# Performance work log

Measured on AMD Instinct MI355X. Metric: run time of the kernel, lower is better.

Reference implementation:

```python
import jax, jax.numpy as jnp
import numpy as np

B, N, E, D, H, C, FF, NQ, NCLS = 4, 1024, 512, 256, 2, 128, 1024, 4, 24
K_LOCAL, K_GLOBAL = 8, 7


def _ln(x, g, b, eps=1e-5):
    m = jnp.mean(x, -1, keepdims=True)
    v = jnp.mean((x - m) ** 2, -1, keepdims=True)
    return (x - m) * jax.lax.rsqrt(v + eps) * g + b


def _knn_mask(dist, k, exclude_self):
    # dist: [n, n]; returns bool mask[target, source] of k nearest sources per target
    n = dist.shape[-1]
    d = jnp.where(jnp.eye(n, dtype=bool), 1e9, dist) if exclude_self else dist
    idx = jax.lax.top_k(-d, k)[1]  # [n, k]
    rows = jnp.arange(n)[:, None]
    return jnp.zeros((n, n), dtype=bool).at[rows, idx].set(True)


def _mha(q, k, v, scale, extra_mask=None):
    # q: [B,Lq,H,C]  k,v: [B,Lk,H,C]
    logits = jnp.einsum('bqhc,bkhc->bhqk', q, k) * scale
    if extra_mask is not None:
        logits = logits + extra_mask
    a = jax.nn.softmax(logits, axis=-1)
    return jnp.einsum('bhqk,bkhc->bqhc', a, v)


def _forward(inputs, cellposes, sparse_rand, emb_W, emb_b, pe_tab, pe_W1, pe_b1, pe_W2, pe_b2,
             gat_W, gat_att_src, gat_att_dst, gat_b, ln_g, ln_b,
             tf_qkv_W, tf_qkv_b, tf_out_W, tf_out_b, tf_ff1_W, tf_ff1_b, tf_ff2_W, tf_ff2_b,
             tf_ln1_g, tf_ln1_b, tf_ln2_g, tf_ln2_b,
             query_embed, pool_in_W, pool_in_b, pool_out_W, pool_out_b,
             m1_W, m1_b, m_ln1_g, m_ln1_b, m2_W, m2_b, m_ln2_g, m_ln2_b, m3_W, m3_b,
             c1_W, c1_b, c2_W, c2_b, c3_W, c3_b, c4_W, c4_b, masks):
    # masks are all ones (full bags) -> key_padding_mask is all-False, no padding effect
    x = inputs @ emb_W.T + emb_b                                  # [B,N,D]
    # 2D position embedding: per-coordinate Embedding -> Linear -> ReLU -> Linear
    pos_idx = jnp.clip(cellposes, 0, 1000).astype(jnp.int32)      # [B,N,2]
    pes = []
    for c in range(2):
        e = pe_tab[c][pos_idx[..., c]]                            # [B,N,D//2]
        e = jax.nn.relu(e @ pe_W1[c].T + pe_b1[c]) @ pe_W2[c].T + pe_b2[c]
        pes.append(e)
    x = x + jnp.concatenate(pes, axis=-1)
    # kNN graph: local k=8 with self-loops + global k=7 without; coalesce('max') => edge-set union
    pm = cellposes.mean(axis=1, keepdims=True)
    ps = cellposes.std(axis=1, keepdims=True) + 1e-8
    pn = (cellposes - pm) / ps
    sq = jnp.sum((pn[:, :, None, :] - pn[:, None, :, :]) ** 2, axis=-1)
    dist = jax.lax.stop_gradient(jnp.sqrt(sq + 1e-12))            # [B,N,N]
    local = jax.vmap(lambda d: _knn_mask(d, K_LOCAL, False))(dist)
    glob = jax.vmap(lambda d: _knn_mask(d, K_GLOBAL, True))(dist)
    adj = local | glob                                            # [B, target, source]
    # GAT layers (PyG GATConv; edge weights are ignored since edge_dim=None)
    for l in range(gat_W.shape[0]):
        res = x
        h = (x @ gat_W[l].T).reshape(B, N, H, C)
        a_src = jnp.einsum('bnhc,hc->bnh', h, gat_att_src[l])
        a_dst = jnp.einsum('bnhc,hc->bnh', h, gat_att_dst[l])
        e = jax.nn.leaky_relu(a_dst[:, :, None, :] + a_src[:, None, :, :], 0.2)  # [B,t,s,H]
        e = jnp.where(adj[..., None], e, -1e9)
        a = jax.nn.softmax(e, axis=2)
        out = jnp.einsum('btsh,bshc->bthc', a, h).reshape(B, N, D) + gat_b[l]
        x = _ln(out + res, ln_g, ln_b)
    # TransformerEncoder: post-norm, ReLU FFN, batch_first, eval (no dropout)
    scale = 1.0 / jnp.sqrt(jnp.float32(C))
    for l in range(tf_qkv_W.shape[0]):
        qkv = x @ tf_qkv_W[l].T + tf_qkv_b[l]
        q, k, v = [t.reshape(B, N, H, C) for t in jnp.split(qkv, 3, axis=-1)]
        o = _mha(q, k, v, scale).reshape(B, N, D) @ tf_out_W[l].T + tf_out_b[l]
        x = _ln(x + o, tf_ln1_g[l], tf_ln1_b[l])
        ff = jax.nn.relu(x @ tf_ff1_W[l].T + tf_ff1_b[l]) @ tf_ff2_W[l].T + tf_ff2_b[l]
        x = _ln(x + ff, tf_ln2_g[l], tf_ln2_b[l])
    x = _ln(x, ln_g, ln_b)
    pooled_avg = x.mean(axis=1)                                   # AdaptiveAvgPool1d(1) == mean over seq
    # Sparse multihead attention pooling with learned queries
    queries = jnp.broadcast_to(query_embed[None], (B, NQ, D))
    attn_mask = jnp.where(sparse_rand < 0.3, 0.0, -1e9)           # [NQ, N]
    Wq, Wk, Wv = jnp.split(pool_in_W, 3, axis=0)
    bq, bk, bv = jnp.split(pool_in_b, 3, axis=0)
    q = (queries @ Wq.T + bq).reshape(B, NQ, H, C)
    k = (x @ Wk.T + bk).reshape(B, N, H, C)
    v = (x @ Wv.T + bv).reshape(B, N, H, C)
    pooled_att = _mha(q, k, v, scale, attn_mask[None, None]).reshape(B, NQ, D) @ pool_out_W.T + pool_out_b
    combined = jnp.concatenate([pooled_avg, pooled_att.reshape(B, NQ * D)], axis=-1)  # [B,(1+NQ)*D]
    h = jax.nn.relu(combined @ m1_W.T + m1_b)
    h = _ln(h, m_ln1_g, m_ln1_b)
    h = jax.nn.relu(h @ m2_W.T + m2_b)
    h = _ln(h, m_ln2_g, m_ln2_b)
    h = h @ m3_W.T + m3_b
    h = jax.nn.relu(h @ c1_W.T + c1_b)
    h = jax.nn.relu(h @ c2_W.T + c2_b)
    h = jax.nn.relu(h @ c3_W.T + c3_b)
    return h @ c4_W.T + c4_b                                      # [B, num_classes]


def setup_inputs() -> dict:
    key = jax.random.key(0)
    ks = iter(jax.random.split(key, 80))
    def W(shape, s=0.02):
        return jax.random.normal(next(ks), shape, jnp.float32) * s
    z = lambda *s: jnp.zeros(s, jnp.float32)
    o = lambda *s: jnp.ones(s, jnp.float32)
    return dict(
        inputs=jax.random.normal(next(ks), (B, N, E), jnp.float32),
        cellposes=jax.random.uniform(next(ks), (B, N, 2), jnp.float32) * 1000.0,
        sparse_rand=jax.random.uniform(next(ks), (NQ, N), jnp.float32),
        emb_W=W((D, E)), emb_b=z(D),
        pe_tab=W((2, 1001, D // 2)), pe_W1=W((2, D // 2, D // 2)), pe_b1=z(2, D // 2),
        pe_W2=W((2, D // 2, D // 2)), pe_b2=z(2, D // 2),
        gat_W=W((2, D, D)), gat_att_src=W((2, H, C)), gat_att_dst=W((2, H, C)), gat_b=z(2, D),
        ln_g=o(D), ln_b=z(D),
        tf_qkv_W=W((2, 3 * D, D)), tf_qkv_b=z(2, 3 * D), tf_out_W=W((2, D, D)), tf_out_b=z(2, D),
        tf_ff1_W=W((2, FF, D)), tf_ff1_b=z(2, FF), tf_ff2_W=W((2, D, FF)), tf_ff2_b=z(2, D),
        tf_ln1_g=o(2, D), tf_ln1_b=z(2, D), tf_ln2_g=o(2, D), tf_ln2_b=z(2, D),
        query_embed=W((NQ, D)),
        pool_in_W=W((3 * D, D)), pool_in_b=z(3 * D), pool_out_W=W((D, D)), pool_out_b=z(D),
        m1_W=W((1024, (1 + NQ) * D)), m1_b=z(1024), m_ln1_g=o(1024), m_ln1_b=z(1024),
        m2_W=W((1024, 1024)), m2_b=z(1024), m_ln2_g=o(1024), m_ln2_b=z(1024),
        m3_W=W((1024, 1024)), m3_b=z(1024),
        c1_W=W((1032, 1024)), c1_b=z(1032), c2_W=W((512, 1032)), c2_b=z(512),
        c3_W=W((256, 512)), c3_b=z(256), c4_W=W((NCLS, 256)), c4_b=z(NCLS),
        masks=jnp.ones((B, N), jnp.int32),
    )


def reference(inputs, cellposes, sparse_rand, emb_W, emb_b, pe_tab, pe_W1, pe_b1, pe_W2, pe_b2,
              gat_W, gat_att_src, gat_att_dst, gat_b, ln_g, ln_b,
              tf_qkv_W, tf_qkv_b, tf_out_W, tf_out_b, tf_ff1_W, tf_ff1_b, tf_ff2_W, tf_ff2_b,
              tf_ln1_g, tf_ln1_b, tf_ln2_g, tf_ln2_b,
              query_embed, pool_in_W, pool_in_b, pool_out_W, pool_out_b,
              m1_W, m1_b, m_ln1_g, m_ln1_b, m2_W, m2_b, m_ln2_g, m_ln2_b, m3_W, m3_b,
              c1_W, c1_b, c2_W, c2_b, c3_W, c3_b, c4_W, c4_b, masks):
    return _forward(inputs, cellposes, sparse_rand, emb_W, emb_b, pe_tab, pe_W1, pe_b1, pe_W2, pe_b2,
                    gat_W, gat_att_src, gat_att_dst, gat_b, ln_g, ln_b,
                    tf_qkv_W, tf_qkv_b, tf_out_W, tf_out_b, tf_ff1_W, tf_ff1_b, tf_ff2_W, tf_ff2_b,
                    tf_ln1_g, tf_ln1_b, tf_ln2_g, tf_ln2_b,
                    query_embed, pool_in_W, pool_in_b, pool_out_W, pool_out_b,
                    m1_W, m1_b, m_ln1_g, m_ln1_b, m2_W, m2_b, m_ln2_g, m_ln2_b, m3_W, m3_b,
                    c1_W, c1_b, c2_W, c2_b, c3_W, c3_b, c4_W, c4_b, masks)
```

## Files before the change

### kernel.cpp

```cpp
#include <hip/hip_runtime.h>
#include <hip/hip_bf16.h>


typedef __bf16 bf16x8 __attribute__((ext_vector_type(8)));
typedef float  f32x4  __attribute__((ext_vector_type(4)));

__device__ __forceinline__ ushort f2b(float f) {
  __hip_bfloat16 h = __float2bfloat16(f);
  return *(ushort*)&h;
}
__device__ __forceinline__ float b2f(ushort u) {
  union { unsigned i; float f; } v; v.i = ((unsigned)u) << 16; return v.f;
}

__device__ __forceinline__ float blk_sum256(float v, float* red) {
  int t = threadIdx.x;
  red[t] = v; __syncthreads();
  #pragma unroll
  for (int off = 128; off > 0; off >>= 1) {
    if (t < off) red[t] += red[t + off];
    __syncthreads();
  }
  float r = red[0]; __syncthreads();
  return r;
}

__device__ __forceinline__ void stage8(const ushort* __restrict__ src, ushort* dst) {
  *(uint4*)dst = *(const uint4*)src;
}
__device__ __forceinline__ void stage8(const float* __restrict__ src, ushort* dst) {
  float4 a = ((const float4*)src)[0];
  float4 b = ((const float4*)src)[1];
  ushort4 o0, o1;
  o0.x = f2b(a.x); o0.y = f2b(a.y); o0.z = f2b(a.z); o0.w = f2b(a.w);
  o1.x = f2b(b.x); o1.y = f2b(b.y); o1.z = f2b(b.z); o1.w = f2b(b.w);
  *(ushort4*)dst = o0;
  *(ushort4*)(dst + 4) = o1;
}

template<typename CT, typename AT, typename WT, bool VSPLIT, bool GATS, bool AMERGE>
__global__ __launch_bounds__(256) void mfma_gemm(
    const AT* __restrict__ A, int lda,
    const WT* __restrict__ Bw, int ldb,
    const float* __restrict__ bias,
    CT* __restrict__ C, int ldc, int K, int relu,
    ushort* __restrict__ VT,
    const float* __restrict__ asrcW, const float* __restrict__ adstW,
    float* __restrict__ ASRC, float* __restrict__ ADST,
    const float* __restrict__ Mp, const float* __restrict__ Lp)
{
  __shared__ ushort As[64][40];
  __shared__ ushort Bs[128][40];
  int tid = threadIdx.x;
  int lane = tid & 63, wave = tid >> 6;
  int wm = wave >> 1, wn = wave & 1;
  int quad = lane >> 4, l16 = lane & 15;
  long mBase = blockIdx.y * 64, nBase = blockIdx.x * 128;

  float aw0 = 0.f, aw1 = 0.f, ainv = 0.f;
  int ap_lrow = 0, ap_qt = 0, ap_b = 0;
  if constexpr (AMERGE) {
    int r = tid >> 2;
    long gm = mBase + r;
    ap_b = (int)(gm >> 10);
    int nn = (int)(gm & 1023);
    ap_qt = nn >> 6;
    ap_lrow = nn & 63;
  }

  f32x4 zero4 = {0.f, 0.f, 0.f, 0.f};
  f32x4 acc[2][4];
  #pragma unroll
  for (int i = 0; i < 2; i++)
    #pragma unroll
    for (int j = 0; j < 4; j++) acc[i][j] = zero4;

  for (int k0 = 0; k0 < K; k0 += 32) {
    if constexpr (AMERGE) {
      int r = tid >> 2, sg = (tid & 3) * 8;
      int col = k0 + sg;
      int hh = col >> 7, cc = col & 127;
      int bh = ap_b * 2 + hh;
      int p0 = (ap_qt * 2 + 0) * 8 + bh;
      int p1 = (ap_qt * 2 + 1) * 8 + bh;
      float m0 = Mp[p0 * 64 + ap_lrow], m1 = Mp[p1 * 64 + ap_lrow];
      float l0 = Lp[p0 * 64 + ap_lrow], l1 = Lp[p1 * 64 + ap_lrow];
      float mm2 = fmaxf(m0, m1);
      float w0 = expf(m0 - mm2), w1 = expf(m1 - mm2);
      float inv = 1.f / (w0 * l0 + w1 * l1);
      const ushort* o0 = (const ushort*)A + ((long)(p0 * 64 + ap_lrow)) * 128 + cc;
      const ushort* o1 = (const ushort*)A + ((long)(p1 * 64 + ap_lrow)) * 128 + cc;
      ushort* dst = &As[r][sg];
      #pragma unroll
      for (int i = 0; i < 8; i++)
        dst[i] = f2b((w0 * b2f(o0[i]) + w1 * b2f(o1[i])) * inv);
    } else {
      int r = tid >> 2, sg = (tid & 3) * 8;
      stage8(A + (mBase + r) * lda + k0 + sg, &As[r][sg]);
    }
    #pragma unroll
    for (int p = 0; p < 2; p++) {
      int idx = p * 256 + tid;
      int r = idx >> 2, sg = (idx & 3) * 8;
      stage8(Bw + (nBase + r) * ldb + k0 + sg, &Bs[r][sg]);
    }
    __syncthreads();
    bf16x8 af[2], bfr[4];
    #pragma unroll
    for (int i = 0; i < 2; i++)
      af[i] = *(const bf16x8*)&As[wm * 32 + i * 16 + l16][quad * 8];
    #pragma unroll
    for (int j = 0; j < 4; j++)
      bfr[j] = *(const bf16x8*)&Bs[wn * 64 + j * 16 + l16][quad * 8];
    #pragma unroll
    for (int i = 0; i < 2; i++)
      #pragma unroll
      for (int j = 0; j < 4; j++)
        acc[i][j] = __builtin_amdgcn_mfma_f32_16x16x32_bf16(af[i], bfr[j], acc[i][j], 0, 0, 0);
    __syncthreads();
  }
  #pragma unroll
  for (int i = 0; i < 2; i++) {
    #pragma unroll
    for (int j = 0; j < 4; j++) {
      long col = nBase + wn * 64 + j * 16 + l16;
      float bv = bias ? bias[col] : 0.f;
      long row0 = mBase + wm * 32 + i * 16 + quad * 4;
      if (VSPLIT && col >= 512) {
        int cm = (int)col - 512, hh = cm >> 7, cc = cm & 127;
        long bidx = row0 >> 10, n0 = row0 & 1023;
        ushort4 o;
        o.x = f2b(acc[i][j][0] + bv);
        o.y = f2b(acc[i][j][1] + bv);
        o.z = f2b(acc[i][j][2] + bv);
        o.w = f2b(acc[i][j][3] + bv);
        *(ushort4*)&VT[(((bidx * 2 + hh) * 128 + cc) << 10) + n0] = o;
      } else {
        #pragma unroll
        for (int r = 0; r < 4; r++) {
          float v = acc[i][j][r] + bv;
          if (relu) v = fmaxf(v, 0.f);
          if constexpr (sizeof(CT) == 2) C[(row0 + r) * ldc + col] = f2b(v);
          else                           C[(row0 + r) * ldc + col] = v;
        }
      }
    }
  }
  if constexpr (GATS) {
    __shared__ float RS[64][2], RD[64][2];
    float ps[2][4], pd[2][4];
    #pragma unroll
    for (int i = 0; i < 2; i++)
      #pragma unroll
      for (int r = 0; r < 4; r++) { ps[i][r] = 0.f; pd[i][r] = 0.f; }
    #pragma unroll
    for (int j = 0; j < 4; j++) {
      long col = nBase + wn * 64 + j * 16 + l16;
      float ws = asrcW[col], wd = adstW[col];
      #pragma unroll
      for (int i = 0; i < 2; i++)
        #pragma unroll
        for (int r = 0; r < 4; r++) {
          ps[i][r] += acc[i][j][r] * ws;
          pd[i][r] += acc[i][j][r] * wd;
        }
    }
    #pragma unroll
    for (int off = 1; off < 16; off <<= 1)
      #pragma unroll
      for (int i = 0; i < 2; i++)
        #pragma unroll
        for (int r = 0; r < 4; r++) {
          ps[i][r] += __shfl_xor(ps[i][r], off);
          pd[i][r] += __shfl_xor(pd[i][r], off);
        }
    if (l16 == 0) {
      #pragma unroll
      for (int i = 0; i < 2; i++)
        #pragma unroll
        for (int r = 0; r < 4; r++) {
          int row = wm * 32 + i * 16 + quad * 4 + r;
          RS[row][wn] = ps[i][r];
          RD[row][wn] = pd[i][r];
        }
    }
    __syncthreads();
    if (tid < 64) {
      long gr = mBase + tid;
      ASRC[gr * 2 + blockIdx.x] = RS[tid][0] + RS[tid][1];
      ADST[gr * 2 + blockIdx.x] = RD[tid][0] + RD[tid][1];
    }
  }
}

template<typename CT, typename AT, typename WT>
static void mgemm(hipStream_t st, const AT* A, int lda, const WT* B, int ldb,
                  const float* bias, CT* C, int ldc, int M, int N, int K, int relu) {
  dim3 grid(N / 128, M / 64);
  mfma_gemm<CT, AT, WT, false, false, false><<<grid, 256, 0, st>>>(
      A, lda, B, ldb, bias, C, ldc, K, relu,
      nullptr, nullptr, nullptr, nullptr, nullptr, nullptr, nullptr);
}
template<typename AT, typename WT>
static void mgemm_vt(hipStream_t st, const AT* A, int lda, const WT* B, int ldb,
                     const float* bias, ushort* C, int ldc, int M, int N, int K, ushort* VT) {
  dim3 grid(N / 128, M / 64);
  mfma_gemm<ushort, AT, WT, true, false, false><<<grid, 256, 0, st>>>(
      A, lda, B, ldb, bias, C, ldc, K, 0, VT,
      nullptr, nullptr, nullptr, nullptr, nullptr, nullptr);
}
template<typename AT, typename WT>
static void mgemm_gat(hipStream_t st, const AT* A, int lda, const WT* B, int ldb,
                      float* C, int ldc, int M, int N, int K,
                      const float* asrcW, const float* adstW, float* AS, float* AD) {
  dim3 grid(N / 128, M / 64);
  mfma_gemm<float, AT, WT, false, true, false><<<grid, 256, 0, st>>>(
      A, lda, B, ldb, nullptr, C, ldc, K, 0, nullptr,
      asrcW, adstW, AS, AD, nullptr, nullptr);
}
template<typename WT>
static void mgemm_amrg(hipStream_t st, const ushort* OP, const float* Mp, const float* Lp,
                       const WT* B, int ldb, const float* bias,
                       float* C, int ldc, int M, int N, int K) {
  dim3 grid(N / 128, M / 64);
  mfma_gemm<float, ushort, WT, false, false, true><<<grid, 256, 0, st>>>(
      OP, 0, B, ldb, bias, C, ldc, K, 0, nullptr,
      nullptr, nullptr, nullptr, nullptr, Mp, Lp);
}

__global__ __launch_bounds__(256) void pos_mlp(
    const float* __restrict__ cellp, const float* __restrict__ tab,
    const float* __restrict__ W1, const float* __restrict__ b1,
    const float* __restrict__ W2, const float* __restrict__ b2,
    float* __restrict__ X, ushort* __restrict__ Xb)
{
  __shared__ ushort Es[64][136];
  __shared__ ushort Bs[128][136];
  __shared__ ushort H1s[64][136];
  int tid = threadIdx.x;
  int lane = tid & 63, wave = tid >> 6;
  int wm = wave >> 1, wn = wave & 1;
  int quad = lane >> 4, l16 = lane & 15;
  int r0 = blockIdx.x * 64, c = blockIdx.y;

  #pragma unroll
  for (int p = 0; p < 4; p++) {
    int idx = p * 256 + tid;
    int r = idx >> 4, c8 = (idx & 15) * 8;
    float pos = cellp[(r0 + r) * 2 + c];
    pos = fminf(fmaxf(pos, 0.f), 1000.f);
    int pi = (int)pos;
    stage8(tab + ((long)(c * 1001 + pi)) * 128 + c8, &Es[r][c8]);
  }
  #pragma unroll
  for (int p = 0; p < 8; p++) {
    int idx = p * 256 + tid;
    int r = idx >> 4, c8 = (idx & 15) * 8;
    stage8(W1 + ((long)(c * 128 + r)) * 128 + c8, &Bs[r][c8]);
  }
  __syncthreads();

  f32x4 zero4 = {0.f, 0.f, 0.f, 0.f};
  f32x4 acc[2][4];
  #pragma unroll
  for (int i = 0; i < 2; i++)
    #pragma unroll
    for (int j = 0; j < 4; j++) acc[i][j] = zero4;
  #pragma unroll
  for (int ks = 0; ks < 4; ks++) {
    bf16x8 af[2], bfr[4];
    #pragma unroll
    for (int i = 0; i < 2; i++)
      af[i] = *(const bf16x8*)&Es[wm * 32 + i * 16 + l16][ks * 32 + quad * 8];
    #pragma unroll
    for (int j = 0; j < 4; j++)
      bfr[j] = *(const bf16x8*)&Bs[wn * 64 + j * 16 + l16][ks * 32 + quad * 8];
    #pragma unroll
    for (int i = 0; i < 2; i++)
      #pragma unroll
      for (int j = 0; j < 4; j++)
        acc[i][j] = __builtin_amdgcn_mfma_f32_16x16x32_bf16(af[i], bfr[j], acc[i][j], 0, 0, 0);
  }
  #pragma unroll
  for (int i = 0; i < 2; i++)
    #pragma unroll
    for (int j = 0; j < 4; j++) {
      int col = wn * 64 + j * 16 + l16;
      float bv = b1[c * 128 + col];
      #pragma unroll
      for (int r = 0; r < 4; r++) {
        int row = wm * 32 + i * 16 + quad * 4 + r;
        H1s[row][col] = f2b(fmaxf(acc[i][j][r] + bv, 0.f));
      }
    }
  __syncthreads();
  #pragma unroll
  for (int p = 0; p < 8; p++) {
    int idx = p * 256 + tid;
    int r = idx >> 4, c8 = (idx & 15) * 8;
    stage8(W2 + ((long)(c * 128 + r)) * 128 + c8, &Bs[r][c8]);
  }
  __syncthreads();
  #pragma unroll
  for (int i = 0; i < 2; i++)
    #pragma unroll
    for (int j = 0; j < 4; j++) acc[i][j] = zero4;
  #pragma unroll
  for (int ks = 0; ks < 4; ks++) {
    bf16x8 af[2], bfr[4];
    #pragma unroll
    for (int i = 0; i < 2; i++)
      af[i] = *(const bf16x8*)&H1s[wm * 32 + i * 16 + l16][ks * 32 + quad * 8];
    #pragma unroll
    for (int j = 0; j < 4; j++)
      bfr[j] = *(const bf16x8*)&Bs[wn * 64 + j * 16 + l16][ks * 32 + quad * 8];
    #pragma unroll
    for (int i = 0; i < 2; i++)
      #pragma unroll
      for (int j = 0; j < 4; j++)
        acc[i][j] = __builtin_amdgcn_mfma_f32_16x16x32_bf16(af[i], bfr[j], acc[i][j], 0, 0, 0);
  }
  #pragma unroll
  for (int i = 0; i < 2; i++)
    #pragma unroll
    for (int j = 0; j < 4; j++) {
      int col = wn * 64 + j * 16 + l16;
      float bv = b2[c * 128 + col];
      #pragma unroll
      for (int r = 0; r < 4; r++) {
        long row = r0 + wm * 32 + i * 16 + quad * 4 + r;
        long idx = row * 256 + c * 128 + col;
        float v = X[idx] + (acc[i][j][r] + bv);
        X[idx] = v;
        Xb[idx] = f2b(v);
      }
    }
}

template<int M_>
__global__ __launch_bounds__(256) void skinny_gemm(
    const float* __restrict__ A, int lda,
    const float* __restrict__ W, int K,
    float* __restrict__ P, int N, int slice)
{
  __shared__ float Asl[M_ * 192];
  __shared__ float Pr[4][M_][64];
  int tid = threadIdx.x;
  int ks = blockIdx.y;
  int kbeg = ks * slice;
  int kend = min(K, kbeg + slice);
  int sl = kend - kbeg;
  for (int idx = tid; idx < M_ * sl; idx += 256) {
    int m = idx / sl, k = idx - m * sl;
    Asl[m * sl + k] = A[(long)m * lda + kbeg + k];
  }
  __syncthreads();
  int n = blockIdx.x * 64 + (tid & 63);
  int sub = tid >> 6;
  int sl4 = (sl + 3) >> 2;
  int k0 = kbeg + sub * sl4;
  int k1 = min(kend, k0 + sl4);
  float acc[M_];
  #pragma unroll
  for (int m = 0; m < M_; m++) acc[m] = 0.f;
  if (n < N) {
    const float* wr = W + (long)n * K;
    for (int k = k0; k < k1; k++) {
      float w = wr[k];
      int kl = k - kbeg;
      #pragma unroll
      for (int m = 0; m < M_; m++) acc[m] += w * Asl[m * sl + kl];
    }
  }
  #pragma unroll
  for (int m = 0; m < M_; m++) Pr[sub][m][tid & 63] = acc[m];
  __syncthreads();
  if (sub == 0 && n < N) {
    #pragma unroll
    for (int m = 0; m < M_; m++) {
      float s = Pr[0][m][tid] + Pr[1][m][tid] + Pr[2][m][tid] + Pr[3][m][tid];
      P[((long)(ks * M_ + m)) * N + n] = s;
    }
  }
}

__global__ __launch_bounds__(256) void skinny_epi(
    const float* __restrict__ P, const float* __restrict__ bias,
    float* __restrict__ out, int M, int N, int KS, int relu)
{
  int idx = blockIdx.x * 256 + threadIdx.x;
  if (idx >= M * N) return;
  int m = idx / N, n = idx - m * N;
  float s = bias[n];
  for (int ks = 0; ks < KS; ks++) s += P[((long)(ks * M + m)) * N + n];
  if (relu) s = fmaxf(s, 0.f);
  out[(long)m * N + n] = s;
}

template<int M_>
static void sgemm(hipStream_t st, const float* A, int lda, const float* W, int K,
                  const float* bias, float* out, float* P, int N, int KS, int relu) {
  int slice = (K + KS - 1) / KS;
  dim3 grid((N + 63) / 64, KS);
  skinny_gemm<M_><<<grid, 256, 0, st>>>(A, lda, W, K, P, N, slice);
  skinny_epi<<<(M_ * N + 255) / 256, 256, 0, st>>>(P, bias, out, M_, N, KS, relu);
}

__global__ __launch_bounds__(256) void bag_stats(const float* __restrict__ cp, float* __restrict__ PN) {
  int b = blockIdx.x, tid = threadIdx.x;
  __shared__ float red[256];
  for (int c = 0; c < 2; c++) {
    float s = 0.f;
    for (int n = tid; n < 1024; n += 256) s += cp[((b << 10) + n) * 2 + c];
    float mean = blk_sum256(s, red) * (1.f / 1024.f);
    s = 0.f;
    for (int n = tid; n < 1024; n += 256) { float d = cp[((b << 10) + n) * 2 + c] - mean; s += d * d; }
    float var = blk_sum256(s, red) * (1.f / 1024.f);
    float inv = 1.f / (sqrtf(var) + 1e-8f);
    for (int n = tid; n < 1024; n += 256)
      PN[((b << 10) + n) * 2 + c] = (cp[((b << 10) + n) * 2 + c] - mean) * inv;
  }
}

__global__ __launch_bounds__(256) void knn_sel(const float* __restrict__ PN,
                                               int* __restrict__ NBR) {
  int blk = blockIdx.x;
  int b = blk >> 7, grp = blk & 127;
  int tid = threadIdx.x;
  int wave = tid >> 6, lane = tid & 63;
  __shared__ float px[1024], py[1024];
  for (int i = tid; i < 1024; i += 256) {
    px[i] = PN[((b << 10) + i) * 2 + 0];
    py[i] = PN[((b << 10) + i) * 2 + 1];
  }
  __syncthreads();
  #pragma unroll
  for (int sub = 0; sub < 2; sub++) {
    int t = grp * 8 + wave * 2 + sub;
    float tx = px[t], ty = py[t];
    float dloc[16];
    #pragma unroll
    for (int k = 0; k < 16; k++) {
      int s = lane + (k << 6);
      float dx = __fadd_rn(px[s], -tx), dy = __fadd_rn(py[s], -ty);
      float d2 = __fadd_rn(__fadd_rn(__fmul_rn(dx, dx), __fmul_rn(dy, dy)), 1e-12f);
      dloc[k] = sqrtf(d2);
    }
    int res[8];
    #pragma unroll
    for (int it = 0; it < 8; it++) {
      float bd = dloc[0]; int bk = 0;
      #pragma unroll
      for (int k = 1; k < 16; k++)
        if (dloc[k] < bd) { bd = dloc[k]; bk = k; }
      unsigned long long key =
          (((unsigned long long)__float_as_uint(bd)) << 32) | (unsigned)(lane + (bk << 6));
      #pragma unroll
      for (int off = 1; off < 64; off <<= 1) {
        unsigned long long o = __shfl_xor(key, off);
        if (o < key) key = o;
      }
      int widx = (int)(key & 0xffffffffu);
      res[it] = widx;
      if ((widx & 63) == lane) dloc[widx >> 6] = 3.4e38f;
    }
    if (lane < 8) NBR[((long)((b << 10) + t)) * 8 + lane] = res[lane];
  }
}

__global__ __launch_bounds__(256) void gat_aggr_ln(
    const float* __restrict__ Hh, const float* __restrict__ ASRC, const float* __restrict__ ADST,
    const int* __restrict__ NBR, const float* __restrict__ gbias,
    const float* __restrict__ lng, const float* __restrict__ lnb,
    float* __restrict__ X, ushort* __restrict__ Xb)
{
  int row = blockIdx.x, tid = threadIdx.x;
  int b = row >> 10;
  __shared__ int nb[8];
  __shared__ float w[2][8];
  __shared__ float red[256];
  if (tid < 8) {
    int v = NBR[(long)row * 8 + tid];
    nb[tid] = min(max(v, 0), 1023);
  }
  __syncthreads();
  if (tid < 16) {
    int i = tid & 7, h = tid >> 3;
    float e = ADST[row * 2 + h] + ASRC[((b << 10) + nb[i]) * 2 + h];
    w[h][i] = (e >= 0.f) ? e : 0.2f * e;
  }
  __syncthreads();
  if (tid < 2) {
    float m = -3.4e38f;
    for (int i = 0; i < 8; i++) m = fmaxf(m, w[tid][i]);
    float s = 0.f;
    for (int i = 0; i < 8; i++) { float e = expf(w[tid][i] - m); w[tid][i] = e; s += e; }
    float inv = 1.f / s;
    for (int i = 0; i < 8; i++) w[tid][i] *= inv;
  }
  __syncthreads();
  int h = tid >> 7, c = tid & 127;
  float acc = 0.f;
  #pragma unroll
  for (int i = 0; i < 8; i++)
    acc += w[h][i] * Hh[((long)((b << 10) + nb[i])) * 256 + h * 128 + c];
  float v = acc + gbias[tid] + X[(long)row * 256 + tid];
  float mean = blk_sum256(v, red) * (1.f / 256.f);
  float dv = v - mean;
  float var = blk_sum256(dv * dv, red) * (1.f / 256.f);
  float o = dv * rsqrtf(var + 1e-5f) * lng[tid] + lnb[tid];
  X[(long)row * 256 + tid] = o;
  Xb[(long)row * 256 + tid] = f2b(o);
}

__global__ __launch_bounds__(256) void add_ln4(const float* __restrict__ res,
    const float* __restrict__ Yv, const float* __restrict__ g, const float* __restrict__ b,
    float* __restrict__ out, ushort* __restrict__ outb)
{
  int wave = threadIdx.x >> 6, lane = threadIdx.x & 63;
  long row = blockIdx.x * 4 + wave;
  const float* yr = Yv + row * 256;
  const float* rr = res ? res + row * 256 : nullptr;
  float v[4];
  float s = 0.f;
  #pragma unroll
  for (int i = 0; i < 4; i++) {
    int d = lane + i * 64;
    float x = yr[d];
    if (rr) x += rr[d];
    v[i] = x; s += x;
  }
  #pragma unroll
  for (int off = 32; off > 0; off >>= 1) s += __shfl_xor(s, off);
  float mean = s * (1.f / 256.f);
  float vs = 0.f;
  #pragma unroll
  for (int i = 0; i < 4; i++) { float dv = v[i] - mean; vs += dv * dv; }
  #pragma unroll
  for (int off = 32; off > 0; off >>= 1) vs += __shfl_xor(vs, off);
  float rstd = rsqrtf(vs * (1.f / 256.f) + 1e-5f);
  #pragma unroll
  for (int i = 0; i < 4; i++) {
    int d = lane + i * 64;
    float o = (v[i] - mean) * rstd * g[d] + b[d];
    out[row * 256 + d] = o;
    if (outb) outb[row * 256 + d] = f2b(o);
  }
}

__global__ __launch_bounds__(256) void add_ln_big(const float* __restrict__ Yv,
    const float* __restrict__ g, const float* __restrict__ b,
    float* __restrict__ out)
{
  int row = blockIdx.x, tid = threadIdx.x;
  __shared__ float red[256];
  float vals[4];
  float s = 0.f;
  #pragma unroll
  for (int i = 0; i < 4; i++) {
    int d = tid + (i << 8);
    float v = Yv[(long)row * 1024 + d];
    vals[i] = v; s += v;
  }
  float mean = blk_sum256(s, red) * (1.f / 1024.f);
  s = 0.f;
  #pragma unroll
  for (int i = 0; i < 4; i++) { float dv = vals[i] - mean; s += dv * dv; }
  float var = blk_sum256(s, red) * (1.f / 1024.f);
  float rstd = rsqrtf(var + 1e-5f);
  #pragma unroll
  for (int i = 0; i < 4; i++) {
    int d = tid + (i << 8);
    out[(long)row * 1024 + d] = (vals[i] - mean) * rstd * g[d] + b[d];
  }
}

__global__ __launch_bounds__(256) void flash_part(const ushort* __restrict__ QKV,
                                                  const ushort* __restrict__ VT,
                                                  ushort* __restrict__ OP,
                                                  float* __restrict__ Mp,
                                                  float* __restrict__ Lp)
{
  const float scale = 0.08838834764831845f;
  int blk = blockIdx.x;
  int bh = blk & 7, rest = blk >> 3;
  int half = rest & 1, qt = rest >> 1;
  int b = bh >> 1, h = bh & 1;
  const ushort* qkg = QKV + (long)b * 1024 * 768 + h * 128;
  const ushort* vtg = VT + ((long)bh << 17);

  __shared__ ushort Qs[64][136];
  __shared__ ushort Ks[64][136];
  __shared__ ushort Vt[128][72];
  __shared__ ushort Ps[4][16][72];

  int tid = threadIdx.x;
  int wave = tid >> 6, lane = tid & 63;
  int quad = lane >> 4, l16 = lane & 15;

  #pragma unroll
  for (int p = 0; p < 4; p++) {
    int idx = p * 256 + tid;
    int r = idx >> 4, c8 = (idx & 15) * 8;
    *(uint4*)&Qs[r][c8] = *(const uint4*)(qkg + (long)(qt * 64 + r) * 768 + c8);
  }
  __syncthreads();
  bf16x8 af[4];
  #pragma unroll
  for (int ks = 0; ks < 4; ks++)
    af[ks] = *(const bf16x8*)&Qs[wave * 16 + l16][ks * 32 + quad * 8];

  f32x4 Oacc[8];
  f32x4 zero4 = {0.f, 0.f, 0.f, 0.f};
  #pragma unroll
  for (int j = 0; j < 8; j++) Oacc[j] = zero4;
  float mr[4], lr[4];
  #pragma unroll
  for (int r = 0; r < 4; r++) { mr[r] = -3.4e38f; lr[r] = 0.f; }

  int kt0 = half * 8;
  for (int kt = kt0; kt < kt0 + 8; kt++) {
    __syncthreads();
    #pragma unroll
    for (int p = 0; p < 4; p++) {
      int idx = p * 256 + tid;
      int r = idx >> 4, c8 = (idx & 15) * 8;
      *(uint4*)&Ks[r][c8] = *(const uint4*)(qkg + (long)(kt * 64 + r) * 768 + 256 + c8);
      int c = idx >> 3, k8 = (idx & 7) * 8;
      *(uint4*)&Vt[c][k8] = *(const uint4*)(vtg + ((long)c << 10) + kt * 64 + k8);
    }
    __syncthreads();
    f32x4 acc[4];
    #pragma unroll
    for (int j = 0; j < 4; j++) acc[j] = zero4;
    #pragma unroll
    for (int ks = 0; ks < 4; ks++) {
      #pragma unroll
      for (int j = 0; j < 4; j++) {
        bf16x8 kb = *(const bf16x8*)&Ks[j * 16 + l16][ks * 32 + quad * 8];
        acc[j] = __builtin_amdgcn_mfma_f32_16x16x32_bf16(af[ks], kb, acc[j], 0, 0, 0);
      }
    }
    float sv[4][4], tmax[4];
    #pragma unroll
    for (int r = 0; r < 4; r++) tmax[r] = -3.4e38f;
    #pragma unroll
    for (int j = 0; j < 4; j++)
      #pragma unroll
      for (int r = 0; r < 4; r++) {
        float x = acc[j][r] * scale;
        sv[j][r] = x;
        tmax[r] = fmaxf(tmax[r], x);
      }
    #pragma unroll
    for (int off = 1; off < 16; off <<= 1)
      #pragma unroll
      for (int r = 0; r < 4; r++) tmax[r] = fmaxf(tmax[r], __shfl_xor(tmax[r], off));
    float alpha[4], rsum[4];
    #pragma unroll
    for (int r = 0; r < 4; r++) {
      float mn = fmaxf(mr[r], tmax[r]);
      alpha[r] = expf(mr[r] - mn);
      mr[r] = mn;
      rsum[r] = 0.f;
    }
    #pragma unroll
    for (int j = 0; j < 4; j++)
      #pragma unroll
      for (int r = 0; r < 4; r++) {
        float p = expf(sv[j][r] - mr[r]);
        sv[j][r] = p;
        rsum[r] += p;
      }
    #pragma unroll
    for (int off = 1; off < 16; off <<= 1)
      #pragma unroll
      for (int r = 0; r < 4; r++) rsum[r] += __shfl_xor(rsum[r], off);
    #pragma unroll
    for (int r = 0; r < 4; r++) lr[r] = lr[r] * alpha[r] + rsum[r];
    #pragma unroll
    for (int j = 0; j < 4; j++)
      #pragma unroll
      for (int r = 0; r < 4; r++)
        Ps[wave][quad * 4 + r][j * 16 + l16] = f2b(sv[j][r]);
    #pragma unroll
    for (int jj = 0; jj < 8; jj++)
      #pragma unroll
      for (int r = 0; r < 4; r++) Oacc[jj][r] *= alpha[r];
    __syncthreads();
    #pragma unroll
    for (int s = 0; s < 2; s++) {
      bf16x8 pa = *(const bf16x8*)&Ps[wave][l16][s * 32 + quad * 8];
      #pragma unroll
      for (int jj = 0; jj < 8; jj++) {
        bf16x8 vb = *(const bf16x8*)&Vt[jj * 16 + l16][s * 32 + quad * 8];
        Oacc[jj] = __builtin_amdgcn_mfma_f32_16x16x32_bf16(pa, vb, Oacc[jj], 0, 0, 0);
      }
    }
  }
  long pbase = (long)blk * 64;
  #pragma unroll
  for (int jj = 0; jj < 8; jj++) {
    int col = jj * 16 + l16;
    #pragma unroll
    for (int r = 0; r < 4; r++) {
      int lrow = wave * 16 + quad * 4 + r;
      OP[(pbase + lrow) * 128 + col] = f2b(Oacc[jj][r]);
    }
  }
  if (l16 == 0) {
    #pragma unroll
    for (int r = 0; r < 4; r++) {
      int lrow = wave * 16 + quad * 4 + r;
      Mp[pbase + lrow] = mr[r];
      Lp[pbase + lrow] = lr[r];
    }
  }
}

__global__ __launch_bounds__(128) void pool_split(
    const float* __restrict__ qe, const float* __restrict__ pinW, const float* __restrict__ pinB,
    const float* __restrict__ srand, const ushort* __restrict__ KV,
    float* __restrict__ PM, float* __restrict__ PL, float* __restrict__ PO)
{
  int cid = blockIdx.x;
  int id = blockIdx.y;
  int h = id & 1, nq = (id >> 1) & 3, b = id >> 3;
  int tid = threadIdx.x;
  __shared__ float qs[128];
  __shared__ float eg[128];
  __shared__ float red[128];
  {
    float a = pinB[h * 128 + tid];
    const float* wr = pinW + ((long)(h * 128 + tid)) * 256;
    const float* qr = qe + nq * 256;
    for (int i = 0; i < 256; i++) a += qr[i] * wr[i];
    qs[tid] = a;
  }
  __syncthreads();
  const float scale = 0.08838834764831845f;
  int s = cid * 128 + tid;
  float d = 0.f;
  {
    const ushort* kr = KV + ((long)((b << 10) + s)) * 512 + h * 128;
    #pragma unroll
    for (int c8 = 0; c8 < 128; c8 += 8) {
      uint4 kv4 = *(const uint4*)(kr + c8);
      const ushort* kp = (const ushort*)&kv4;
      #pragma unroll
      for (int j = 0; j < 8; j++) d += qs[c8 + j] * b2f(kp[j]);
    }
  }
  float lg = d * scale + ((srand[nq * 1024 + s] < 0.3f) ? 0.f : -1e9f);
  red[tid] = lg; __syncthreads();
  for (int off = 64; off > 0; off >>= 1) { if (tid < off) red[tid] = fmaxf(red[tid], red[tid + off]); __syncthreads(); }
  float m = red[0]; __syncthreads();
  float e = expf(lg - m);
  eg[tid] = e;
  red[tid] = e; __syncthreads();
  for (int off = 64; off > 0; off >>= 1) { if (tid < off) red[tid] += red[tid + off]; __syncthreads(); }
  float l = red[0];
  __syncthreads();
  float o = 0.f;
  const ushort* vbase = KV + ((long)((b << 10) + cid * 128)) * 512 + 256 + h * 128 + tid;
  for (int ss = 0; ss < 128; ss++)
    o += eg[ss] * b2f(vbase[(long)ss * 512]);
  int part = id * 8 + cid;
  PO[(long)part * 128 + tid] = o;
  if (tid == 0) { PM[part] = m; PL[part] = l; }
}

__global__ __launch_bounds__(128) void pool_merge(
    const float* __restrict__ PM, const float* __restrict__ PL, const float* __restrict__ PO,
    float* __restrict__ ATTP)
{
  int id = blockIdx.x;
  int h = id & 1, nq = (id >> 1) & 3, b = id >> 3;
  int tid = threadIdx.x;
  float m = -3.4e38f;
  #pragma unroll
  for (int c = 0; c < 8; c++) m = fmaxf(m, PM[id * 8 + c]);
  float l = 0.f, o = 0.f;
  #pragma unroll
  for (int c = 0; c < 8; c++) {
    float w = expf(PM[id * 8 + c] - m);
    l += PL[id * 8 + c] * w;
    o += PO[(long)(id * 8 + c) * 128 + tid] * w;
  }
  ATTP[(b * 4 + nq) * 256 + h * 128 + tid] = o / l;
}

__global__ __launch_bounds__(256) void col_mean_part(const float* __restrict__ X,
                                                     float* __restrict__ PSUM)
{
  int blk = blockIdx.x;
  int b = blk >> 4, ch = blk & 15;
  int d = threadIdx.x;
  float s = 0.f;
  int n0 = ch * 64;
  const float* xr = X + ((long)((b << 10) + n0)) * 256 + d;
  #pragma unroll 4
  for (int n = 0; n < 64; n++) s += xr[(long)n * 256];
  PSUM[(long)blk * 256 + d] = s;
}

__global__ __launch_bounds__(256) void combined_merge(const float* __restrict__ PSUM,
    const float* __restrict__ ATTO, float* __restrict__ CMB)
{
  int b = blockIdx.x, d = threadIdx.x;
  float s = 0.f;
  #pragma unroll
  for (int ch = 0; ch < 16; ch++) s += PSUM[(long)(b * 16 + ch) * 256 + d];
  CMB[b * 1280 + d] = s * (1.f / 1024.f);
  #pragma unroll
  for (int q = 0; q < 4; q++)
    CMB[b * 1280 + 256 + q * 256 + d] = ATTO[(b * 4 + q) * 256 + d];
}

__global__ void fill_out_zero(float* __restrict__ dst, int n) {
  int i = blockIdx.x * blockDim.x + threadIdx.x;
  if (i < n) dst[i] = 0.f;
}

extern "C" void kernel_launch(void* const* d_in, const int* in_sizes, int n_in,
                              void* d_out, int out_size, void* d_ws, size_t ws_size,
                              hipStream_t stream)
{
  const float* inp      = (const float*)d_in[0];
  const float* cellp    = (const float*)d_in[1];
  const float* srand    = (const float*)d_in[2];
  const float* emb_W    = (const float*)d_in[3];
  const float* emb_b    = (const float*)d_in[4];
  const float* pe_tab   = (const float*)d_in[5];
  const float* pe_W1    = (const float*)d_in[6];
  const float* pe_b1    = (const float*)d_in[7];
  const float* pe_W2    = (const float*)d_in[8];
  const float* pe_b2    = (const float*)d_in[9];
  const float* gat_W    = (const float*)d_in[10];
  const float* gat_asrc = (const float*)d_in[11];
  const float* gat_adst = (const float*)d_in[12];
  const float* gat_b    = (const float*)d_in[13];
  const float* ln_g     = (const float*)d_in[14];
  const float* ln_b     = (const float*)d_in[15];
  const float* qkv_W    = (const float*)d_in[16];
  const float* qkv_b    = (const float*)d_in[17];
  const float* out_W    = (const float*)d_in[18];
  const float* out_b    = (const float*)d_in[19];
  const float* ff1_W    = (const float*)d_in[20];
  const float* ff1_b    = (const float*)d_in[21];
  const float* ff2_W    = (const float*)d_in[22];
  const float* ff2_b    = (const float*)d_in[23];
  const float* ln1_g    = (const float*)d_in[24];
  const float* ln1_b    = (const float*)d_in[25];
  const float* ln2_g    = (const float*)d_in[26];
  const float* ln2_b    = (const float*)d_in[27];
  const float* q_emb    = (const float*)d_in[28];
  const float* pin_W    = (const float*)d_in[29];
  const float* pin_b    = (const float*)d_in[30];
  const float* pout_W   = (const float*)d_in[31];
  const float* pout_b   = (const float*)d_in[32];
  const float* m1_W     = (const float*)d_in[33];
  const float* m1_b     = (const float*)d_in[34];
  const float* mln1_g   = (const float*)d_in[35];
  const float* mln1_b   = (const float*)d_in[36];
  const float* m2_W     = (const float*)d_in[37];
  const float* m2_b     = (const float*)d_in[38];
  const float* mln2_g   = (const float*)d_in[39];
  const float* mln2_b   = (const float*)d_in[40];
  const float* m3_W     = (const float*)d_in[41];
  const float* m3_b     = (const float*)d_in[42];
  const float* c1_W     = (const float*)d_in[43];
  const float* c1_b     = (const float*)d_in[44];
  const float* c2_W     = (const float*)d_in[45];
  const float* c2_b     = (const float*)d_in[46];
  const float* c3_W     = (const float*)d_in[47];
  const float* c3_b     = (const float*)d_in[48];
  const float* c4_W     = (const float*)d_in[49];
  const float* c4_b     = (const float*)d_in[50];
  (void)in_sizes; (void)n_in;

  char* base = (char*)d_ws;
  size_t off = 0;
  auto alloc = [&](size_t bytes) { void* p = base + off; off += (bytes + 255) & ~size_t(255); return p; };
  float* PN    = (float*)alloc(32768);
  float* AS    = (float*)alloc(32768);
  float* AD    = (float*)alloc(32768);
  float* ATTP  = (float*)alloc(16384);
  float* ATTO  = (float*)alloc(16384);
  float* CMB   = (float*)alloc(20480);
  float* Ha    = (float*)alloc(16384);
  float* Hb    = (float*)alloc(16384);
  float* Hc    = (float*)alloc(16640);
  float* Hd    = (float*)alloc(8192);
  float* He    = (float*)alloc(4096);
  float* Pk    = (float*)alloc(262144);
  float* PPM   = (float*)alloc(1024);
  float* PPL   = (float*)alloc(1024);
  float* PPO   = (float*)alloc(131072);
  float* PSUM  = (float*)alloc(65536);
  int*   NBR   = (int*)alloc(131072);
  float* X     = (float*)alloc(4194304);
  ushort* Xb   = (ushort*)alloc(2097152);
  char*  Rq    = (char*)alloc(6291456);
  char*  Rf    = (char*)alloc(4194304);
  float*  F1   = (float*)alloc(4194304);
  ushort* QKVb = (ushort*)Rq;
  float*  F2   = (float*)Rq;
  ushort* KVb  = (ushort*)Rq;
  ushort* VT   = (ushort*)(Rf + 2097152);
  ushort* FFBb = (ushort*)Rf;
  ushort* OPrt = (ushort*)F1;
  float*  Mprt = Pk;
  float*  Lprt = Pk + 16384;
  if (ws_size < off) { fill_out_zero<<<1, 128, 0, stream>>>((float*)d_out, out_size); return; }

  bag_stats<<<4, 256, 0, stream>>>(cellp, PN);
  knn_sel<<<512, 256, 0, stream>>>(PN, NBR);

  mgemm<float>(stream, inp, 512, emb_W, 512, emb_b, X, 256, 4096, 256, 512, 0);
  pos_mlp<<<dim3(64, 2), 256, 0, stream>>>(cellp, pe_tab, pe_W1, pe_b1, pe_W2, pe_b2, X, Xb);

  for (int l = 0; l < 2; l++) {
    mgemm_gat(stream, Xb, 256, gat_W + l * 65536, 256, F1, 256, 4096, 256, 256,
              gat_asrc + l * 256, gat_adst + l * 256, AS, AD);
    gat_aggr_ln<<<4096, 256, 0, stream>>>(F1, AS, AD, NBR, gat_b + l * 256, ln_g, ln_b, X, Xb);
  }

  for (int l = 0; l < 2; l++) {
    mgemm_vt(stream, Xb, 256, qkv_W + (long)l * 768 * 256, 256, qkv_b + l * 768,
             QKVb, 768, 4096, 768, 256, VT);
    flash_part<<<256, 256, 0, stream>>>(QKVb, VT, OPrt, Mprt, Lprt);
    mgemm_amrg(stream, OPrt, Mprt, Lprt, out_W + l * 65536, 256, out_b + l * 256,
               F2, 256, 4096, 256, 256);
    add_ln4<<<1024, 256, 0, stream>>>(X, F2, ln1_g + l * 256, ln1_b + l * 256, X, Xb);
    mgemm<ushort>(stream, Xb, 256, ff1_W + l * 262144, 256, ff1_b + l * 1024,
                  FFBb, 1024, 4096, 1024, 256, 1);
    mgemm<float>(stream, FFBb, 1024, ff2_W + l * 262144, 1024, ff2_b + l * 256,
                 F2, 256, 4096, 256, 1024, 0);
    add_ln4<<<1024, 256, 0, stream>>>(X, F2, ln2_g + l * 256, ln2_b + l * 256, X, Xb);
  }

  add_ln4<<<1024, 256, 0, stream>>>((const float*)nullptr, X, ln_g, ln_b, X, Xb);

  mgemm<ushort>(stream, Xb, 256, pin_W + 65536, 256, pin_b + 256, KVb, 512, 4096, 512, 256, 0);
  pool_split<<<dim3(8, 32), 128, 0, stream>>>(q_emb, pin_W, pin_b, srand, KVb, PPM, PPL, PPO);
  pool_merge<<<32, 128, 0, stream>>>(PPM, PPL, PPO, ATTP);
  sgemm<16>(stream, ATTP, 256, pout_W, 256, pout_b, ATTO, Pk, 256, 2, 0);
  col_mean_part<<<64, 256, 0, stream>>>(X, PSUM);
  combined_merge<<<4, 256, 0, stream>>>(PSUM, ATTO, CMB);

  sgemm<4>(stream, CMB, 1280, m1_W, 1280, m1_b, Ha, Pk, 1024, 8, 1);
  add_ln_big<<<4, 256, 0, stream>>>(Ha, mln1_g, mln1_b, Ha);
  sgemm<4>(stream, Ha, 1024, m2_W, 1024, m2_b, Hb, Pk, 1024, 8, 1);
  add_ln_big<<<4, 256, 0, stream>>>(Hb, mln2_g, mln2_b, Hb);
  sgemm<4>(stream, Hb, 1024, m3_W, 1024, m3_b, Ha, Pk, 1024, 8, 0);
  sgemm<4>(stream, Ha, 1024, c1_W, 1024, c1_b, Hc, Pk, 1032, 8, 1);
  sgemm<4>(stream, Hc, 1032, c2_W, 1032, c2_b, Hd, Pk, 512, 8, 1);
  sgemm<4>(stream, Hd, 512, c3_W, 512, c3_b, He, Pk, 256, 4, 1);
  sgemm<4>(stream, He, 256, c4_W, 256, c4_b, (float*)d_out, Pk, 24, 2, 0);
}
```

Baseline: 594.1 us.

## Fuse split-K reduction, bias, ReLU and LayerNorm into next skinny GEMM prologue

The head MLP chain used to run a separate epilogue kernel after each split-K skinny GEMM, plus standalone LayerNorm kernels. Now each following skinny GEMM reduces the previous partial sums, adds bias, applies ReLU and, where needed, LayerNorm in its prologue, and partial buffers ping-pong between two workspaces. This removes about ten small kernel launches and their intermediate round trips. In exchange, every block redundantly recomputes the reduction, including a full 1024-wide LayerNorm per block in the LN mode.

Result: slower. 705.2 us (+18.7%).

```diff
diff --git a/kernel.cpp b/kernel.cpp
--- a/kernel.cpp
+++ b/kernel.cpp
@@ -57,7 +57,6 @@
   int quad = lane >> 4, l16 = lane & 15;
   long mBase = blockIdx.y * 64, nBase = blockIdx.x * 128;
 
-  float aw0 = 0.f, aw1 = 0.f, ainv = 0.f;
   int ap_lrow = 0, ap_qt = 0, ap_b = 0;
   if constexpr (AMERGE) {
     int r = tid >> 2;
@@ -337,22 +336,65 @@
     }
 }
 
-template<int M_>
+template<int M_, int AMODE>
 __global__ __launch_bounds__(256) void skinny_gemm(
     const float* __restrict__ A, int lda,
     const float* __restrict__ W, int K,
-    float* __restrict__ P, int N, int slice)
+    float* __restrict__ P, int N, int slice,
+    const float* __restrict__ pP, const float* __restrict__ pBias,
+    int pKS, int pRelu,
+    const float* __restrict__ lnG, const float* __restrict__ lnB)
 {
   __shared__ float Asl[M_ * 192];
   __shared__ float Pr[4][M_][64];
+  __shared__ float red[256];
+  __shared__ float Vrow[(AMODE == 2) ? M_ * 1024 : 1];
   int tid = threadIdx.x;
   int ks = blockIdx.y;
   int kbeg = ks * slice;
   int kend = min(K, kbeg + slice);
   int sl = kend - kbeg;
+
+  if constexpr (AMODE == 2) {
+    for (int m = 0; m < M_; m++) {
+      float vloc[4];
+      float s = 0.f;
+      #pragma unroll
+      for (int i = 0; i < 4; i++) {
+        int d = tid + (i << 8);
+        float v = pBias[d];
+        for (int kk = 0; kk < pKS; kk++) v += pP[((long)(kk * M_ + m)) * K + d];
+        if (pRelu) v = fmaxf(v, 0.f);
+        vloc[i] = v; s += v;
+      }
+      float mean = blk_sum256(s, red) * (1.f / 1024.f);
+      s = 0.f;
+      #pragma unroll
+      for (int i = 0; i < 4; i++) { float dv = vloc[i] - mean; s += dv * dv; }
+      float var = blk_sum256(s, red) * (1.f / 1024.f);
+      float rstd = rsqrtf(var + 1e-5f);
+      #pragma unroll
+      for (int i = 0; i < 4; i++) {
+        int d = tid + (i << 8);
+        Vrow[m * 1024 + d] = (vloc[i] - mean) * rstd * lnG[d] + lnB[d];
+      }
+    }
+    __syncthreads();
+  }
+
   for (int idx = tid; idx < M_ * sl; idx += 256) {
     int m = idx / sl, k = idx - m * sl;
-    Asl[m * sl + k] = A[(long)m * lda + kbeg + k];
+    if constexpr (AMODE == 0) {
+      Asl[m * sl + k] = A[(long)m * lda + kbeg + k];
+    } else if constexpr (AMODE == 1) {
+      int col = kbeg + k;
+      float v = pBias[col];
+      for (int kk = 0; kk < pKS; kk++) v += pP[((long)(kk * M_ + m)) * K + col];
+      if (pRelu) v = fmaxf(v, 0.f);
+      Asl[m * sl + k] = v;
+    } else {
+      Asl[m * sl + k] = Vrow[m * 1024 + kbeg + k];
+    }
   }
   __syncthreads();
   int n = blockIdx.x * 64 + (tid & 63);
@@ -395,15 +437,6 @@
   for (int ks = 0; ks < KS; ks++) s += P[((long)(ks * M + m)) * N + n];
   if (relu) s = fmaxf(s, 0.f);
   out[(long)m * N + n] = s;
-}
-
-template<int M_>
-static void sgemm(hipStream_t st, const float* A, int lda, const float* W, int K,
-                  const float* bias, float* out, float* P, int N, int KS, int relu) {
-  int slice = (K + KS - 1) / KS;
-  dim3 grid((N + 63) / 64, KS);
-  skinny_gemm<M_><<<grid, 256, 0, st>>>(A, lda, W, K, P, N, slice);
-  skinny_epi<<<(M_ * N + 255) / 256, 256, 0, st>>>(P, bias, out, M_, N, KS, relu);
 }
 
 __global__ __launch_bounds__(256) void bag_stats(const float* __restrict__ cp, float* __restrict__ PN) {
@@ -545,33 +578,6 @@
     float o = (v[i] - mean) * rstd * g[d] + b[d];
     out[row * 256 + d] = o;
     if (outb) outb[row * 256 + d] = f2b(o);
-  }
-}
-
-__global__ __launch_bounds__(256) void add_ln_big(const float* __restrict__ Yv,
-    const float* __restrict__ g, const float* __restrict__ b,
-    float* __restrict__ out)
-{
-  int row = blockIdx.x, tid = threadIdx.x;
-  __shared__ float red[256];
-  float vals[4];
-  float s = 0.f;
-  #pragma unroll
-  for (int i = 0; i < 4; i++) {
-    int d = tid + (i << 8);
-    float v = Yv[(long)row * 1024 + d];
-    vals[i] = v; s += v;
-  }
-  float mean = blk_sum256(s, red) * (1.f / 1024.f);
-  s = 0.f;
-  #pragma unroll
-  for (int i = 0; i < 4; i++) { float dv = vals[i] - mean; s += dv * dv; }
-  float var = blk_sum256(s, red) * (1.f / 1024.f);
-  float rstd = rsqrtf(var + 1e-5f);
-  #pragma unroll
-  for (int i = 0; i < 4; i++) {
-    int d = tid + (i << 8);
-    out[(long)row * 1024 + d] = (vals[i] - mean) * rstd * g[d] + b[d];
   }
 }
 
@@ -888,12 +894,8 @@
   float* ATTP  = (float*)alloc(16384);
   float* ATTO  = (float*)alloc(16384);
   float* CMB   = (float*)alloc(20480);
-  float* Ha    = (float*)alloc(16384);
-  float* Hb    = (float*)alloc(16384);
-  float* Hc    = (float*)alloc(16640);
-  float* Hd    = (float*)alloc(8192);
-  float* He    = (float*)alloc(4096);
   float* Pk    = (float*)alloc(262144);
+  float* PkH   = (float*)alloc(266240);
   float* PPM   = (float*)alloc(1024);
   float* PPL   = (float*)alloc(1024);
   float* PPO   = (float*)alloc(131072);
@@ -912,6 +914,8 @@
   ushort* OPrt = (ushort*)F1;
   float*  Mprt = Pk;
   float*  Lprt = Pk + 16384;
+  float*  Pa   = PkH;
+  float*  Pb   = PkH + 33024;
   if (ws_size < off) { fill_out_zero<<<1, 128, 0, stream>>>((float*)d_out, out_size); return; }
 
   bag_stats<<<4, 256, 0, stream>>>(cellp, PN);
@@ -945,17 +949,36 @@
   mgemm<ushort>(stream, Xb, 256, pin_W + 65536, 256, pin_b + 256, KVb, 512, 4096, 512, 256, 0);
   pool_split<<<dim3(8, 32), 128, 0, stream>>>(q_emb, pin_W, pin_b, srand, KVb, PPM, PPL, PPO);
   pool_merge<<<32, 128, 0, stream>>>(PPM, PPL, PPO, ATTP);
-  sgemm<16>(stream, ATTP, 256, pout_W, 256, pout_b, ATTO, Pk, 256, 2, 0);
+  {
+    dim3 g((256 + 63) / 64, 2);
+    skinny_gemm<16, 0><<<g, 256, 0, stream>>>(ATTP, 256, pout_W, 256, Pk, 256, 128,
+                                              nullptr, nullptr, 0, 0, nullptr, nullptr);
+    skinny_epi<<<(16 * 256 + 255) / 256, 256, 0, stream>>>(Pk, pout_b, ATTO, 16, 256, 2, 0);
+  }
   col_mean_part<<<64, 256, 0, stream>>>(X, PSUM);
   combined_merge<<<4, 256, 0, stream>>>(PSUM, ATTO, CMB);
 
-  sgemm<4>(stream, CMB, 1280, m1_W, 1280, m1_b, Ha, Pk, 1024, 8, 1);
-  add_ln_big<<<4, 256, 0, stream>>>(Ha, mln1_g, mln1_b, Ha);
-  sgemm<4>(stream, Ha, 1024, m2_W, 1024, m2_b, Hb, Pk, 1024, 8, 1);
-  add_ln_big<<<4, 256, 0, stream>>>(Hb, mln2_g, mln2_b, Hb);
-  sgemm<4>(stream, Hb, 1024, m3_W, 1024, m3_b, Ha, Pk, 1024, 8, 0);
-  sgemm<4>(stream, Ha, 1024, c1_W, 1024, c1_b, Hc, Pk, 1032, 8, 1);
-  sgemm<4>(stream, Hc, 1032, c2_W, 1032, c2_b, Hd, Pk, 512, 8, 1);
-  sgemm<4>(stream, Hd, 512, c3_W, 512, c3_b, He, Pk, 256, 4, 1);
-  sgemm<4>(stream, He, 256, c4_W, 256, c4_b, (float*)d_out, Pk, 24, 2, 0);
-}
+  {
+    dim3 g1(16, 8);
+    skinny_gemm<4, 0><<<g1, 256, 0, stream>>>(CMB, 1280, m1_W, 1280, Pa, 1024, 160,
+                                              nullptr, nullptr, 0, 0, nullptr, nullptr);
+    dim3 g2(16, 8);
+    skinny_gemm<4, 2><<<g2, 256, 0, stream>>>(nullptr, 0, m2_W, 1024, Pb, 1024, 128,
+                                              Pa, m1_b, 8, 1, mln1_g, mln1_b);
+    skinny_gemm<4, 2><<<g2, 256, 0, stream>>>(nullptr, 0, m3_W, 1024, Pa, 1024, 128,
+                                              Pb, m2_b, 8, 1, mln2_g, mln2_b);
+    dim3 g4(17, 8);
+    skinny_gemm<4, 1><<<g4, 256, 0, stream>>>(nullptr, 0, c1_W, 1024, Pb, 1032, 128,
+                                              Pa, m3_b, 8, 0, nullptr, nullptr);
+    dim3 g5(8, 8);
+    skinny_gemm<4, 1><<<g5, 256, 0, stream>>>(nullptr, 0, c2_W, 1032, Pa, 512, 129,
+                                              Pb, c1_b, 8, 1, nullptr, nullptr);
+    dim3 g6(4, 8);
+    skinny_gemm<4, 1><<<g6, 256, 0, stream>>>(nullptr, 0, c3_W, 512, Pb, 256, 64,
+                                              Pa, c2_b, 8, 1, nullptr, nullptr);
+    dim3 g7(1, 2);
+    skinny_gemm<4, 1><<<g7, 256, 0, stream>>>(nullptr, 0, c4_W, 256, Pa, 24, 128,
+                                              Pb, c3_b, 8, 1, nullptr, nullptr);
+    skinny_epi<<<1, 256, 0, stream>>>(Pa, c4_b, (float*)d_out, 4, 24, 2, 0);
+  }
+}
```
